# Optimization experiments

Measured on AMD Instinct MI355X. Metric: run time of the kernel, lower is better.

Reference implementation:

```python
import jax, jax.numpy as jnp
import numpy as np
import math

NUM_LEVELS = 16
LEVEL_DIM = 2
BASE_RES = 16
MAX_RES = 2048
HASHMAP_SIZE = 1 << 19  # 2**log2_hashmap_size
B, N = 4, 262144


def setup_inputs() -> dict:
    key = jax.random.key(0)
    k1, k2 = jax.random.split(key)
    x = jax.random.uniform(k1, (B, N, 3), dtype=jnp.float32)  # coords in [0,1]
    # per-level hash tables, init uniform(-1e-4, 1e-4) as in the torch module
    embeddings = jax.random.uniform(
        k2, (NUM_LEVELS, HASHMAP_SIZE, LEVEL_DIM),
        minval=-1e-4, maxval=1e-4, dtype=jnp.float32)
    return {"x": x, "embeddings": embeddings}


def reference(x, embeddings):
    # per_level_scale = exp((ln(max)-ln(base))/(L-1))
    per_level_scale = math.exp((math.log(MAX_RES) - math.log(BASE_RES)) / (NUM_LEVELS - 1))
    H = HASHMAP_SIZE
    feats = []
    for level in range(NUM_LEVELS):
        res = int(BASE_RES * per_level_scale ** level)  # static per level
        # floor coords, wrap into [0, res)
        cf = jnp.floor(x * res).astype(jnp.int32) % res  # [B,N,3]
        # hash = (c0 + c1*res + c2*res^2) mod H, computed in modular arithmetic
        # so everything fits in int32 (max term ~2047 * (2^19-1) < 2^31).
        h = (cf[..., 0] % H
             + (cf[..., 1] * res) % H
             + (cf[..., 2] * ((res * res) % H)) % H) % H  # [B,N]
        feats.append(embeddings[level][h])  # gather -> [B,N,LEVEL_DIM]
    return jnp.concatenate(feats, axis=-1)  # [B,N,NUM_LEVELS*LEVEL_DIM]
```

## Files before the change

kernel.cpp:

```cpp
#include <hip/hip_runtime.h>
#include <cmath>

#define NLEVELS 16
#define HSIZE   (1 << 19)
#define HMASK   (HSIZE - 1)

typedef float v2f __attribute__((ext_vector_type(2)));
typedef float v4f __attribute__((ext_vector_type(4)));

struct LevelParams {
    int res[NLEVELS];
    int r2mod[NLEVELS];
};

__device__ __forceinline__ int hash_one(float x0, float x1, float x2, int res, int r2)
{
    const float fr = (float)res;
    int c0 = (int)floorf(x0 * fr); if (c0 >= res) c0 -= res;
    int c1 = (int)floorf(x1 * fr); if (c1 >= res) c1 -= res;
    int c2 = (int)floorf(x2 * fr); if (c2 >= res) c2 -= res;
    return (c0 + ((c1 * res) & HMASK) + ((c2 * r2) & HMASK)) & HMASK;
}

__global__ __launch_bounds__(256)
void hashgrid_gather(const float* __restrict__ x,
                     const float* __restrict__ emb,
                     v2f* __restrict__ ws,
                     LevelParams lp, int npts)
{
    __shared__ float sx[256 * 3];

    const int tid   = threadIdx.x;
    const int g     = blockIdx.x & 7;
    const int chunk = blockIdx.x >> 3;
    const int block_base = chunk * 256;

    const int nfl   = npts * 3;
    const int base3 = block_base * 3;
    #pragma unroll
    for (int k = 0; k < 3; ++k) {
        int idx = base3 + tid + k * 256;
        if (idx < nfl) sx[tid + k * 256] = __builtin_nontemporal_load(&x[idx]);
    }
    __syncthreads();

    const int p = block_base + tid;
    if (p >= npts) return;

    const float x0 = sx[tid * 3 + 0];
    const float x1 = sx[tid * 3 + 1];
    const float x2 = sx[tid * 3 + 2];

    const v2f* __restrict__ e2 = (const v2f*)emb;

    const int lA = g;
    const int lB = 15 - g;

    const int hA = hash_one(x0, x1, x2, lp.res[lA], lp.r2mod[lA]);
    const int hB = hash_one(x0, x1, x2, lp.res[lB], lp.r2mod[lB]);

    const v2f vA = e2[(size_t)lA * HSIZE + hA];
    const v2f vB = e2[(size_t)lB * HSIZE + hB];

    __builtin_nontemporal_store(vA, &ws[(size_t)lA * npts + p]);
    __builtin_nontemporal_store(vB, &ws[(size_t)lB * npts + p]);
}

__global__ __launch_bounds__(256)
void hashgrid_transpose(const v2f* __restrict__ ws,
                        v4f* __restrict__ out4, int npts)
{
    const int t = blockIdx.x * 256 + threadIdx.x;
    const int p = t >> 3;
    const int j = t & 7;
    if (p >= npts) return;

    const v2f a = __builtin_nontemporal_load(&ws[(size_t)(2 * j)     * npts + p]);
    const v2f b = __builtin_nontemporal_load(&ws[(size_t)(2 * j + 1) * npts + p]);

    v4f o; o.x = a.x; o.y = a.y; o.z = b.x; o.w = b.y;
    __builtin_nontemporal_store(o, &out4[(size_t)p * 8 + j]);
}

__global__ __launch_bounds__(256)
void hashgrid_fwd(const float* __restrict__ x,
                  const float* __restrict__ emb,
                  float* __restrict__ out,
                  LevelParams lp, int npts)
{
    __shared__ float sx[256 * 3];
    const int tid        = threadIdx.x;
    const int block_base = blockIdx.x * 256;
    const int nfl        = npts * 3;
    const int base3      = block_base * 3;
    #pragma unroll
    for (int k = 0; k < 3; ++k) {
        int idx = base3 + tid + k * 256;
        if (idx < nfl) sx[tid + k * 256] = x[idx];
    }
    __syncthreads();
    const int p = block_base + tid;
    if (p >= npts) return;
    const float x0 = sx[tid * 3 + 0], x1 = sx[tid * 3 + 1], x2 = sx[tid * 3 + 2];
    const float2* __restrict__ e2 = (const float2*)emb;
    float2 v[NLEVELS];
    #pragma unroll
    for (int l = 0; l < NLEVELS; ++l) {
        const int h = hash_one(x0, x1, x2, lp.res[l], lp.r2mod[l]);
        v[l] = e2[(size_t)l * HSIZE + h];
    }
    float4* __restrict__ o4 = (float4*)(out + (size_t)p * (NLEVELS * 2));
    #pragma unroll
    for (int i = 0; i < 8; ++i)
        o4[i] = make_float4(v[2 * i].x, v[2 * i].y, v[2 * i + 1].x, v[2 * i + 1].y);
}

extern "C" void kernel_launch(void* const* d_in, const int* in_sizes, int n_in,
                              void* d_out, int out_size, void* d_ws, size_t ws_size,
                              hipStream_t stream)
{
    const float* x   = (const float*)d_in[0];
    const float* emb = (const float*)d_in[1];
    float*       out = (float*)d_out;

    const int npts = in_sizes[0] / 3;

    LevelParams lp;
    const double s = std::exp((std::log(2048.0) - std::log(16.0)) / 15.0);
    for (int l = 0; l < NLEVELS; ++l) {
        const double r = 16.0 * std::pow(s, (double)l);
        const int res  = (int)r;
        lp.res[l]   = res;
        lp.r2mod[l] = (int)(((long long)res * res) % HSIZE);
    }

    const size_t ws_need = (size_t)NLEVELS * (size_t)npts * sizeof(v2f);
    if (ws_size >= ws_need) {
        const int chunks  = (npts + 255) / 256;
        const int grid1   = chunks * 8;
        hipLaunchKernelGGL(hashgrid_gather, dim3(grid1), dim3(256), 0, stream,
                           x, emb, (v2f*)d_ws, lp, npts);
        const int grid2 = (npts * 8 + 255) / 256;
        hipLaunchKernelGGL(hashgrid_transpose, dim3(grid2), dim3(256), 0, stream,
                           (const v2f*)d_ws, (v4f*)out, npts);
    } else {
        const int blocks = (npts + 255) / 256;
        hipLaunchKernelGGL(hashgrid_fwd, dim3(blocks), dim3(256), 0, stream,
                           x, emb, out, lp, npts);
    }
}
```

Baseline: 370.3 us.

## Fuse coarse-level gathers into transpose pass and rebalance fine-level gather blocks

Result: faster. 348.3 us (-5.9%).

```diff
diff --git a/kernel.cpp b/kernel.cpp
--- a/kernel.cpp
+++ b/kernel.cpp
@@ -23,63 +23,114 @@
 }
 
 __global__ __launch_bounds__(256)
-void hashgrid_gather(const float* __restrict__ x,
-                     const float* __restrict__ emb,
-                     v2f* __restrict__ ws,
-                     LevelParams lp, int npts)
-{
-    __shared__ float sx[256 * 3];
-
-    const int tid   = threadIdx.x;
-    const int g     = blockIdx.x & 7;
-    const int chunk = blockIdx.x >> 3;
-    const int block_base = chunk * 256;
-
-    const int nfl   = npts * 3;
-    const int base3 = block_base * 3;
+void hashgrid_gather2(const float* __restrict__ x,
+                      const float* __restrict__ emb,
+                      v2f* __restrict__ ws,
+                      LevelParams lp, int npts, int blocksA)
+{
+    __shared__ float sx[768];
+    const int tid = threadIdx.x;
+
+    int level, base, end;
+    if ((int)blockIdx.x < blocksA) {
+        const int g = blockIdx.x & 7;
+        level = 5 + g;
+        base  = (int)(blockIdx.x >> 3) * 256;
+        end   = npts;
+    } else {
+        const int idx = (int)blockIdx.x - blocksA;
+        const int g   = idx & 7;
+        int shard, nsh;
+        if (g < 3)      { level = 13; shard = g;     nsh = 3; }
+        else if (g < 6) { level = 14; shard = g - 3; nsh = 3; }
+        else            { level = 15; shard = g - 6; nsh = 2; }
+        const int shardN = (npts + nsh - 1) / nsh;
+        base = shard * shardN + (idx >> 3) * 256;
+        end  = min(npts, (shard + 1) * shardN);
+        if (base >= end) return;
+    }
+
+    const int nfl = npts * 3;
+    const int b3  = base * 3;
     #pragma unroll
     for (int k = 0; k < 3; ++k) {
-        int idx = base3 + tid + k * 256;
+        const int idx = b3 + tid + k * 256;
         if (idx < nfl) sx[tid + k * 256] = __builtin_nontemporal_load(&x[idx]);
     }
     __syncthreads();
 
-    const int p = block_base + tid;
-    if (p >= npts) return;
-
-    const float x0 = sx[tid * 3 + 0];
-    const float x1 = sx[tid * 3 + 1];
-    const float x2 = sx[tid * 3 + 2];
+    const int p = base + tid;
+    if (p >= end) return;
+
+    const int h = hash_one(sx[tid * 3], sx[tid * 3 + 1], sx[tid * 3 + 2],
+                           lp.res[level], lp.r2mod[level]);
+    const v2f v = ((const v2f*)emb)[(size_t)level * HSIZE + h];
+    __builtin_nontemporal_store(v, &ws[(size_t)level * npts + p]);
+}
+
+__global__ __launch_bounds__(256)
+void hashgrid_finalize(const float* __restrict__ x,
+                       const float* __restrict__ emb,
+                       const v2f* __restrict__ ws,
+                       v4f* __restrict__ out4,
+                       LevelParams lp, int npts)
+{
+    __shared__ float sx[768];
+    __shared__ v2f   sl[11][257];
+
+    const int tid = threadIdx.x;
+    const int p0  = (int)blockIdx.x * 256;
+
+    const int nfl = npts * 3;
+    const int b3  = p0 * 3;
+    #pragma unroll
+    for (int k = 0; k < 3; ++k) {
+        const int idx = b3 + tid + k * 256;
+        if (idx < nfl) sx[tid + k * 256] = __builtin_nontemporal_load(&x[idx]);
+    }
+
+    const int p = p0 + tid;
+    v2f r[11];
+    #pragma unroll
+    for (int li = 0; li < 11; ++li) {
+        r[li] = (p < npts)
+              ? __builtin_nontemporal_load(&ws[(size_t)(5 + li) * npts + p])
+              : (v2f)(0.0f);
+    }
+    #pragma unroll
+    for (int li = 0; li < 11; ++li) sl[li][tid] = r[li];
+    __syncthreads();
 
     const v2f* __restrict__ e2 = (const v2f*)emb;
-
-    const int lA = g;
-    const int lB = 15 - g;
-
-    const int hA = hash_one(x0, x1, x2, lp.res[lA], lp.r2mod[lA]);
-    const int hB = hash_one(x0, x1, x2, lp.res[lB], lp.r2mod[lB]);
-
-    const v2f vA = e2[(size_t)lA * HSIZE + hA];
-    const v2f vB = e2[(size_t)lB * HSIZE + hB];
-
-    __builtin_nontemporal_store(vA, &ws[(size_t)lA * npts + p]);
-    __builtin_nontemporal_store(vB, &ws[(size_t)lB * npts + p]);
-}
-
-__global__ __launch_bounds__(256)
-void hashgrid_transpose(const v2f* __restrict__ ws,
-                        v4f* __restrict__ out4, int npts)
-{
-    const int t = blockIdx.x * 256 + threadIdx.x;
-    const int p = t >> 3;
-    const int j = t & 7;
-    if (p >= npts) return;
-
-    const v2f a = __builtin_nontemporal_load(&ws[(size_t)(2 * j)     * npts + p]);
-    const v2f b = __builtin_nontemporal_load(&ws[(size_t)(2 * j + 1) * npts + p]);
-
-    v4f o; o.x = a.x; o.y = a.y; o.z = b.x; o.w = b.y;
-    __builtin_nontemporal_store(o, &out4[(size_t)p * 8 + j]);
+    const int j  = tid & 7;
+    const int tq = tid >> 3;
+
+    #pragma unroll
+    for (int k = 0; k < 8; ++k) {
+        const int pp = k * 32 + tq;
+        const int pt = p0 + pp;
+        if (pt < npts) {
+            const float x0 = sx[pp * 3 + 0];
+            const float x1 = sx[pp * 3 + 1];
+            const float x2 = sx[pp * 3 + 2];
+            v2f va, vb;
+            if (j == 0) {
+                va = e2[(size_t)0 * HSIZE + hash_one(x0, x1, x2, lp.res[0], lp.r2mod[0])];
+                vb = e2[(size_t)1 * HSIZE + hash_one(x0, x1, x2, lp.res[1], lp.r2mod[1])];
+            } else if (j == 1) {
+                va = e2[(size_t)2 * HSIZE + hash_one(x0, x1, x2, lp.res[2], lp.r2mod[2])];
+                vb = e2[(size_t)3 * HSIZE + hash_one(x0, x1, x2, lp.res[3], lp.r2mod[3])];
+            } else if (j == 2) {
+                va = e2[(size_t)4 * HSIZE + hash_one(x0, x1, x2, lp.res[4], lp.r2mod[4])];
+                vb = sl[0][pp];
+            } else {
+                va = sl[2 * j - 5][pp];
+                vb = sl[2 * j - 4][pp];
+            }
+            v4f o; o.x = va.x; o.y = va.y; o.z = vb.x; o.w = vb.y;
+            __builtin_nontemporal_store(o, &out4[(size_t)p0 * 8 + k * 256 + tid]);
+        }
+    }
 }
 
 __global__ __launch_bounds__(256)
@@ -136,13 +187,15 @@
 
     const size_t ws_need = (size_t)NLEVELS * (size_t)npts * sizeof(v2f);
     if (ws_size >= ws_need) {
-        const int chunks  = (npts + 255) / 256;
-        const int grid1   = chunks * 8;
-        hipLaunchKernelGGL(hashgrid_gather, dim3(grid1), dim3(256), 0, stream,
-                           x, emb, (v2f*)d_ws, lp, npts);
-        const int grid2 = (npts * 8 + 255) / 256;
-        hipLaunchKernelGGL(hashgrid_transpose, dim3(grid2), dim3(256), 0, stream,
-                           (const v2f*)d_ws, (v4f*)out, npts);
+        const int cA      = (npts + 255) / 256;
+        const int blocksA = cA * 8;
+        const int shardN2 = (npts + 1) / 2;
+        const int cB      = (shardN2 + 255) / 256;
+        const int grid1   = blocksA + cB * 8;
+        hipLaunchKernelGGL(hashgrid_gather2, dim3(grid1), dim3(256), 0, stream,
+                           x, emb, (v2f*)d_ws, lp, npts, blocksA);
+        hipLaunchKernelGGL(hashgrid_finalize, dim3(cA), dim3(256), 0, stream,
+                           x, emb, (const v2f*)d_ws, (v4f*)out, lp, npts);
     } else {
         const int blocks = (npts + 255) / 256;
         hipLaunchKernelGGL(hashgrid_fwd, dim3(blocks), dim3(256), 0, stream,
```
